# Kernel tuning notes

Measured on AMD Instinct MI355X. Metric: run time of the kernel, lower is better.

The kernel has to match this reference:

```python
import jax
import jax.numpy as jnp
import numpy as np

T, B = 128, 64
A_DIM, Z_DIM, K_MIX = 32, 64, 16
HIDDEN, NUM_LAYERS = 128, 2
Q_REG = 1e-3
R_REG = 1e-3


def _lstm_layer(x, Wih, Whh, bih, bhh):
    # x: [T, B, in]; torch gate order i, f, g, o
    H = Whh.shape[1]
    h0 = jnp.zeros((x.shape[1], H), x.dtype)

    def step(carry, xt):
        h, c = carry
        gates = xt @ Wih.T + bih + h @ Whh.T + bhh
        i, f, g, o = jnp.split(gates, 4, axis=-1)
        c = jax.nn.sigmoid(f) * c + jax.nn.sigmoid(i) * jnp.tanh(g)
        h = jax.nn.sigmoid(o) * jnp.tanh(c)
        return (h, c), h

    _, hs = jax.lax.scan(step, (h0, h0), x)
    return hs


def _weights(as_, lstm_params, lin_W, lin_b):
    x = as_
    for (Wih, Whh, bih, bhh) in lstm_params:
        x = _lstm_layer(x, Wih, Whh, bih, bhh)
    logits = x @ lin_W.T + lin_b  # [T, B, K]
    return jax.nn.softmax(logits, axis=-1)


def setup_inputs() -> dict:
    key = jax.random.key(0)
    ks = jax.random.split(key, 16)
    inp = {
        "as_": jax.random.normal(ks[0], (T, B, A_DIM), jnp.float32),
        # 0.3 scale keeps the mixture transition matrix spectral radius < 1
        "mat_A_K": 0.3 * jax.random.normal(ks[1], (K_MIX, Z_DIM, Z_DIM), jnp.float32),
        "mat_C_K": jax.random.normal(ks[2], (K_MIX, A_DIM, Z_DIM), jnp.float32),
        "Q_L": jax.random.normal(ks[3], (Z_DIM, Z_DIM), jnp.float32),
        "R_L": jax.random.normal(ks[4], (A_DIM, A_DIM), jnp.float32),
        "lin_W": jax.random.normal(ks[5], (K_MIX, HIDDEN), jnp.float32) / np.sqrt(HIDDEN),
        "lin_b": jnp.zeros((K_MIX,), jnp.float32),
    }
    s = 1.0 / np.sqrt(HIDDEN)
    for l in range(NUM_LAYERS):
        in_dim = A_DIM if l == 0 else HIDDEN
        k1, k2 = jax.random.split(jax.random.fold_in(key, 100 + l))
        inp[f"lstm_Wih{l}"] = s * jax.random.normal(k1, (4 * HIDDEN, in_dim), jnp.float32)
        inp[f"lstm_Whh{l}"] = s * jax.random.normal(k2, (4 * HIDDEN, HIDDEN), jnp.float32)
        inp[f"lstm_bih{l}"] = jnp.zeros((4 * HIDDEN,), jnp.float32)
        inp[f"lstm_bhh{l}"] = jnp.zeros((4 * HIDDEN,), jnp.float32)
    return inp


def reference(as_, mat_A_K, mat_C_K, Q_L, R_L, lin_W, lin_b,
              lstm_Wih0, lstm_Whh0, lstm_bih0, lstm_bhh0,
              lstm_Wih1, lstm_Whh1, lstm_bih1, lstm_bhh1):
    lstm_params = [(lstm_Wih0, lstm_Whh0, lstm_bih0, lstm_bhh0),
                   (lstm_Wih1, lstm_Whh1, lstm_bih1, lstm_bhh1)]
    w = _weights(as_, lstm_params, lin_W, lin_b)            # [T, B, K]
    mat_As = jnp.einsum('tbk,kij->tbij', w, mat_A_K)         # [T, B, z, z]
    mat_Cs = jnp.einsum('tbk,kij->tbij', w, mat_C_K)         # [T, B, a, z]

    I_z = jnp.eye(Z_DIM, dtype=as_.dtype)
    I_a = jnp.eye(A_DIM, dtype=as_.dtype)
    Q = Q_L @ Q_L.T + Q_REG * I_z
    R = R_L @ R_L.T + R_REG * I_a

    mean0 = jnp.zeros((B, Z_DIM, 1), as_.dtype)              # initial_state_mean = 0
    cov0 = jnp.broadcast_to(I_z, (B, Z_DIM, Z_DIM))          # initial_state_covariance = I

    def sym(M):
        return 0.5 * (M + jnp.swapaxes(M, 1, 2))

    def step(carry, inp):
        mean_p, cov_p = carry
        A_t, C_t, a_t = inp                                   # [B,z,z], [B,a,z], [B,a]
        C_tT = jnp.swapaxes(C_t, 1, 2)
        S = C_t @ cov_p @ C_tT + R                            # [B, a, a]
        K_t = cov_p @ C_tT @ jnp.linalg.inv(S)                # [B, z, a]
        mean_t = mean_p + K_t @ (a_t[..., None] - C_t @ mean_p)
        mean_next = A_t @ mean_t
        cov_t = sym(cov_p - K_t @ C_t @ cov_p)
        cov_next = sym(A_t @ cov_t @ jnp.swapaxes(A_t, 1, 2) + Q)
        return (mean_next, cov_next), (mean_t, cov_t, mean_next, cov_next)

    _, (means, covs, next_means, next_covs) = jax.lax.scan(
        step, (mean0, cov0), (mat_As, mat_Cs, as_))
    return means, covs, next_means, next_covs, mat_As, mat_Cs
```

## Files before the change

kernel.cpp:

```cpp
#include <hip/hip_runtime.h>
#include <math.h>

#define T_LEN 128
#define B_SZ  64
#define AD    32
#define ZD    64
#define KMIX  16
#define HID   128

#define WS_B0 106496
#define WS_B1 107008
#define WS_Q  107520
#define WS_R  111616
#define WS_W  112640

#define OUT_MEANS   0
#define OUT_COVS    524288
#define OUT_NMEANS  34078720
#define OUT_NCOVS   34603008
#define OUT_MATA    68157440
#define OUT_MATC    101711872

__device__ __forceinline__ float sigmoidf_(float x){ return 1.0f/(1.0f + expf(-x)); }

__device__ __forceinline__ unsigned short f2bf(float f){
  unsigned u = __float_as_uint(f);
  u += 0x7FFFu + ((u >> 16) & 1u);
  return (unsigned short)(u >> 16);
}

__global__ __launch_bounds__(256) void prep_kernel(
    const float* __restrict__ Wih0, const float* __restrict__ Whh0,
    const float* __restrict__ bih0, const float* __restrict__ bhh0,
    const float* __restrict__ Wih1, const float* __restrict__ Whh1,
    const float* __restrict__ bih1, const float* __restrict__ bhh1,
    const float* __restrict__ QL,   const float* __restrict__ RL,
    float* __restrict__ ws)
{
  int idx = blockIdx.x*256 + threadIdx.x;
  unsigned short* w16 = (unsigned short*)ws;
  if (idx < 212992) {
    const float* src; int local, base, IN;
    if (idx < 16384)       { src = Wih0; local = idx;          base = 0;      IN = 32; }
    else if (idx < 81920)  { src = Whh0; local = idx - 16384;  base = 16384;  IN = 128; }
    else if (idx < 147456) { src = Wih1; local = idx - 81920;  base = 81920;  IN = 128; }
    else                   { src = Whh1; local = idx - 147456; base = 147456; IN = 128; }
    int pair = local >> 10, g = (local >> 1) & 511, lo = local & 1;
    int k = pair*2 + lo;
    w16[base + local] = f2bf(src[g*IN + k]);
  } else if (idx < 213504) {
    int g = idx - 212992; ws[WS_B0 + g] = bih0[g] + bhh0[g];
  } else if (idx < 214016) {
    int g = idx - 213504; ws[WS_B1 + g] = bih1[g] + bhh1[g];
  } else if (idx < 218112) {
    int e = idx - 214016; int i = e >> 6, j = e & 63;
    float s = (i==j) ? 1e-3f : 0.f;
    for (int k = 0; k < 64; ++k) s += QL[i*64+k]*QL[j*64+k];
    ws[WS_Q + e] = s;
  } else if (idx < 219136) {
    int e = idx - 218112; int i = e >> 5, j = e & 31;
    float s = (i==j) ? 1e-3f : 0.f;
    for (int k = 0; k < 32; ++k) s += RL[i*32+k]*RL[j*32+k];
    ws[WS_R + e] = s;
  }
}

__global__ __launch_bounds__(1024) void lstm_kernel(
    const float* __restrict__ as_, const float* __restrict__ ws,
    const float* __restrict__ linW, const float* __restrict__ linb,
    float* __restrict__ wout)
{
  const int b = blockIdx.x, tid = threadIdx.x;
  const int g = tid & 511, hf = tid >> 9;
  const unsigned* W0ih = (const unsigned*)ws;
  const unsigned* W0hh = W0ih + 16*512;
  const unsigned* W1ih = W0hh + 64*512;
  const unsigned* W1hh = W1ih + 64*512;

  __shared__ float xs[2][32];
  __shared__ float h0[128];
  __shared__ float h1[128];
  __shared__ float gpart[2][512];
  __shared__ float lw[16*132];

  for (int e = tid; e < 2048; e += 1024) lw[(e >> 7)*132 + (e & 127)] = linW[e];
  if (tid < 128) { h0[tid] = 0.f; h1[tid] = 0.f; }
  if (tid < 32)  xs[0][tid] = as_[(0*B_SZ + b)*AD + tid];
  float c0 = 0.f, c1 = 0.f;
  const float bias0 = (hf == 0) ? ws[WS_B0 + g] : 0.f;
  const float bias1 = (hf == 0) ? ws[WS_B1 + g] : 0.f;
  const float lbk = linb[tid & 15];
  __syncthreads();

  for (int t = 0; t < T_LEN; ++t) {
    const int cp = t & 1, np = cp ^ 1;
    {
      float acc = bias0;
      const int k0i = hf*8, k0h = hf*32;
      #pragma unroll
      for (int kk = 0; kk < 8; ++kk) {
        const unsigned u = W0ih[(k0i+kk)*512 + g];
        acc += __uint_as_float(u << 16) * xs[cp][2*(k0i+kk)]
             + __uint_as_float(u & 0xFFFF0000u) * xs[cp][2*(k0i+kk)+1];
      }
      #pragma unroll 8
      for (int kk = 0; kk < 32; ++kk) {
        const unsigned u = W0hh[(k0h+kk)*512 + g];
        acc += __uint_as_float(u << 16) * h0[2*(k0h+kk)]
             + __uint_as_float(u & 0xFFFF0000u) * h0[2*(k0h+kk)+1];
      }
      gpart[hf][g] = acc;
    }
    __syncthreads();
    if (tid < 128) {
      float ig = sigmoidf_(gpart[0][tid]     + gpart[1][tid]);
      float fg = sigmoidf_(gpart[0][tid+128] + gpart[1][tid+128]);
      float gg = tanhf    (gpart[0][tid+256] + gpart[1][tid+256]);
      float og = sigmoidf_(gpart[0][tid+384] + gpart[1][tid+384]);
      c0 = fg*c0 + ig*gg;
      h0[tid] = og * tanhf(c0);
    } else if (tid >= 512 && tid < 544 && t+1 < T_LEN) {
      xs[np][tid-512] = as_[((t+1)*B_SZ + b)*AD + (tid-512)];
    }
    __syncthreads();
    {
      float acc = bias1;
      const int k0 = hf*32;
      #pragma unroll 8
      for (int kk = 0; kk < 32; ++kk) {
        const unsigned u = W1ih[(k0+kk)*512 + g];
        acc += __uint_as_float(u << 16) * h0[2*(k0+kk)]
             + __uint_as_float(u & 0xFFFF0000u) * h0[2*(k0+kk)+1];
      }
      #pragma unroll 8
      for (int kk = 0; kk < 32; ++kk) {
        const unsigned u = W1hh[(k0+kk)*512 + g];
        acc += __uint_as_float(u << 16) * h1[2*(k0+kk)]
             + __uint_as_float(u & 0xFFFF0000u) * h1[2*(k0+kk)+1];
      }
      gpart[hf][g] = acc;
    }
    __syncthreads();
    if (tid < 128) {
      float ig = sigmoidf_(gpart[0][tid]     + gpart[1][tid]);
      float fg = sigmoidf_(gpart[0][tid+128] + gpart[1][tid+128]);
      float gg = tanhf    (gpart[0][tid+256] + gpart[1][tid+256]);
      float og = sigmoidf_(gpart[0][tid+384] + gpart[1][tid+384]);
      c1 = fg*c1 + ig*gg;
      h1[tid] = og * tanhf(c1);
    }
    __syncthreads();
    if (tid < 64) {
      const int k = tid & 15, q = tid >> 4;
      float acc = 0.f;
      const float* lr = &lw[k*132 + q*32];
      const float* hr = &h1[q*32];
      #pragma unroll 8
      for (int j = 0; j < 32; ++j) acc += lr[j] * hr[j];
      acc += __shfl_xor(acc, 16);
      acc += __shfl_xor(acc, 32);
      const float logit = acc + lbk;
      float m = logit;
      m = fmaxf(m, __shfl_xor(m, 1));
      m = fmaxf(m, __shfl_xor(m, 2));
      m = fmaxf(m, __shfl_xor(m, 4));
      m = fmaxf(m, __shfl_xor(m, 8));
      const float e = expf(logit - m);
      float s = e;
      s += __shfl_xor(s, 1); s += __shfl_xor(s, 2);
      s += __shfl_xor(s, 4); s += __shfl_xor(s, 8);
      if (tid < 16) wout[(t*B_SZ + b)*KMIX + k] = e / s;
    }
  }
}

__global__ __launch_bounds__(256) void mix_kernel(
    const float* __restrict__ w, const float* __restrict__ AK,
    const float* __restrict__ CK, float* __restrict__ out)
{
  float* matA = out + OUT_MATA;
  float* matC = out + OUT_MATC;
  const int tb0 = blockIdx.x * 16;
  const int tid = threadIdx.x;
  __shared__ float wl[16][16];
  { int lt = tid >> 4, k = tid & 15; wl[lt][k] = w[(tb0 + lt)*16 + k]; }
  __syncthreads();

  for (int e = tid; e < ZD*ZD; e += 256) {
    float v[16];
    #pragma unroll
    for (int u = 0; u < 16; ++u) v[u] = 0.f;
    #pragma unroll 4
    for (int k = 0; k < 16; ++k) {
      float a = AK[k*ZD*ZD + e];
      #pragma unroll
      for (int u = 0; u < 16; ++u) v[u] += wl[u][k] * a;
    }
    #pragma unroll
    for (int u = 0; u < 16; ++u) matA[(size_t)(tb0+u)*(ZD*ZD) + e] = v[u];
  }
  for (int e = tid; e < AD*ZD; e += 256) {
    float v[16];
    #pragma unroll
    for (int u = 0; u < 16; ++u) v[u] = 0.f;
    #pragma unroll 4
    for (int k = 0; k < 16; ++k) {
      float a = CK[k*AD*ZD + e];
      #pragma unroll
      for (int u = 0; u < 16; ++u) v[u] += wl[u][k] * a;
    }
    #pragma unroll
    for (int u = 0; u < 16; ++u) matC[(size_t)(tb0+u)*(AD*ZD) + e] = v[u];
  }
}

__global__ __launch_bounds__(512, 1) void kalman_kernel(
    const float* __restrict__ as_, const float* __restrict__ ws,
    float* __restrict__ out)
{
  const int b = blockIdx.x, tid = threadIdx.x;
  const float* Rm = ws + WS_R;
  const float* Qg = ws + WS_Q;
  const float* matA = out + OUT_MATA;
  const float* matC = out + OUT_MATC;
  float* means  = out + OUT_MEANS;
  float* covs   = out + OUT_COVS;
  float* nmeans = out + OUT_NMEANS;
  float* ncovs  = out + OUT_NCOVS;

  __shared__ __align__(16) float covp[64*68];
  __shared__ __align__(16) float At[2][64*68];
  __shared__ __align__(16) float Cm[2][32*68];
  __shared__ __align__(16) float CPm[32*68];
  __shared__ __align__(16) float Wm[32*68];
  __shared__ float Smat[32*36];
  __shared__ __align__(16) float Um[64*68];
  __shared__ __align__(16) float Vt[32*68];

  for (int e = tid; e < 64*68; e += 512) covp[e] = 0.f;
  __syncthreads();
  for (int e = tid; e < 64*64; e += 512) {
    const int i = e >> 6, j = e & 63;
    covp[i*68 + j] = (i == j) ? 1.f : 0.f;
  }
  float4 qr0, qr1;
  {
    const int i2 = (tid >> 4)*2, j0 = (tid & 15)*4;
    qr0 = *(const float4*)&Qg[(i2+0)*64 + j0];
    qr1 = *(const float4*)&Qg[(i2+1)*64 + j0];
  }
  {
    const float* Ag = matA + (size_t)b*4096;
    const float* Cg = matC + (size_t)b*2048;
    for (int e = tid; e < 4096; e += 512) At[0][(e & 63)*68 + (e >> 6)] = Ag[e];
    for (int e = tid; e < 2048; e += 512) Cm[0][(e >> 6)*68 + (e & 63)] = Cg[e];
  }
  __syncthreads();

  int cur = 0;
  for (int t = 0; t < T_LEN; ++t) {
    const int tb = t*B_SZ + b;
    const int nxt = cur ^ 1;

    if (tid < 256) {
      const int i2 = (tid >> 4)*2, j0 = (tid & 15)*4;
      const bool do64 = ((tid & 15) == 15);
      const float* Cr0 = &Cm[cur][(i2+0)*68];
      const float* Cr1 = &Cm[cur][(i2+1)*68];
      float4 accA = make_float4(0,0,0,0), accB = accA;
      float s64a = 0.f, s64b = 0.f;
      #pragma unroll 4
      for (int k4 = 0; k4 < 16; ++k4) {
        const float4 a4 = *(const float4*)&Cr0[k4*4];
        const float4 c4 = *(const float4*)&Cr1[k4*4];
        const float4 b0 = *(const float4*)&covp[(k4*4+0)*68 + j0];
        const float4 b1 = *(const float4*)&covp[(k4*4+1)*68 + j0];
        const float4 b2 = *(const float4*)&covp[(k4*4+2)*68 + j0];
        const float4 b3 = *(const float4*)&covp[(k4*4+3)*68 + j0];
        accA.x += a4.x*b0.x + a4.y*b1.x + a4.z*b2.x + a4.w*b3.x;
        accA.y += a4.x*b0.y + a4.y*b1.y + a4.z*b2.y + a4.w*b3.y;
        accA.z += a4.x*b0.z + a4.y*b1.z + a4.z*b2.z + a4.w*b3.z;
        accA.w += a4.x*b0.w + a4.y*b1.w + a4.z*b2.w + a4.w*b3.w;
        accB.x += c4.x*b0.x + c4.y*b1.x + c4.z*b2.x + c4.w*b3.x;
        accB.y += c4.x*b0.y + c4.y*b1.y + c4.z*b2.y + c4.w*b3.y;
        accB.z += c4.x*b0.z + c4.y*b1.z + c4.z*b2.z + c4.w*b3.z;
        accB.w += c4.x*b0.w + c4.y*b1.w + c4.z*b2.w + c4.w*b3.w;
        if (do64) {
          const float m0 = covp[(k4*4+0)*68+64], m1 = covp[(k4*4+1)*68+64];
          const float m2 = covp[(k4*4+2)*68+64], m3 = covp[(k4*4+3)*68+64];
          s64a += a4.x*m0 + a4.y*m1 + a4.z*m2 + a4.w*m3;
          s64b += c4.x*m0 + c4.y*m1 + c4.z*m2 + c4.w*m3;
        }
      }
      *(float4*)&CPm[(i2+0)*68 + j0] = accA;
      *(float4*)&CPm[(i2+1)*68 + j0] = accB;
      if (do64) {
        const float2 av = *(const float2*)&as_[(size_t)tb*AD + i2];
        CPm[(i2+0)*68 + 64] = s64a - av.x;
        CPm[(i2+1)*68 + 64] = s64b - av.y;
      }
    }
    __syncthreads();
    if (tid < 256) {
      const int i2 = (tid >> 4)*2, j2 = (tid & 15)*2;
      const float* cpr0 = &CPm[(i2+0)*68];
      const float* cpr1 = &CPm[(i2+1)*68];
      const float* cr0  = &Cm[cur][(j2+0)*68];
      const float* cr1  = &Cm[cur][(j2+1)*68];
      float s00=0,s01=0,s10=0,s11=0;
      #pragma unroll 4
      for (int k4 = 0; k4 < 16; ++k4) {
        const float4 p0 = *(const float4*)&cpr0[k4*4];
        const float4 p1 = *(const float4*)&cpr1[k4*4];
        const float4 c0 = *(const float4*)&cr0[k4*4];
        const float4 c1 = *(const float4*)&cr1[k4*4];
        s00 += p0.x*c0.x + p0.y*c0.y + p0.z*c0.z + p0.w*c0.w;
        s01 += p0.x*c1.x + p0.y*c1.y + p0.z*c1.z + p0.w*c1.w;
        s10 += p1.x*c0.x + p1.y*c0.y + p1.z*c0.z + p1.w*c0.w;
        s11 += p1.x*c1.x + p1.y*c1.y + p1.z*c1.z + p1.w*c1.w;
      }
      Smat[(i2+0)*36 + j2+0] = s00 + Rm[(i2+0)*32 + j2+0];
      Smat[(i2+0)*36 + j2+1] = s01 + Rm[(i2+0)*32 + j2+1];
      Smat[(i2+1)*36 + j2+0] = s10 + Rm[(i2+1)*32 + j2+0];
      Smat[(i2+1)*36 + j2+1] = s11 + Rm[(i2+1)*32 + j2+1];
    }
    __syncthreads();
    {
      const int wv = tid >> 6, lane = tid & 63;
      if (wv == 0) {
        if (lane < 32) {
          float Lr[32];
          float invd = 0.f;
          #pragma unroll
          for (int j = 0; j < 32; ++j) Lr[j] = Smat[lane*36 + j];
          #pragma unroll
          for (int k = 0; k < 32; ++k) {
            const float piv = __shfl(Lr[k], k);
            const float ir  = 1.0f / sqrtf(piv);
            const float lik = Lr[k] * ir;
            invd = (lane == k) ? ir : invd;
            #pragma unroll
            for (int j = k+1; j < 32; ++j) {
              const float ljk = __shfl(lik, j);
              Lr[j] -= lik * ljk;
            }
            Lr[k] = lik;
          }
          #pragma unroll
          for (int j = 0; j < 32; ++j)
            if (j < lane) Smat[lane*36 + j] = Lr[j];
          Smat[lane*36 + lane] = invd;
        }
      } else {
        const int su = tid - 64;
        const int row2 = (su & 31)*2, g = su >> 5;
        const int q0c = g*4, q1c = (g+14)*4;
        const float* Atc = At[cur];
        float4 acc0 = make_float4(0,0,0,0), acc1 = acc0, acc2 = acc0, acc3 = acc0;
        #pragma unroll 8
        for (int k = 0; k < 64; ++k) {
          const float2 a2 = *(const float2*)&Atc[k*68 + row2];
          const float4 b0 = *(const float4*)&covp[k*68 + q0c];
          acc0.x += a2.x*b0.x; acc0.y += a2.x*b0.y; acc0.z += a2.x*b0.z; acc0.w += a2.x*b0.w;
          acc1.x += a2.y*b0.x; acc1.y += a2.y*b0.y; acc1.z += a2.y*b0.z; acc1.w += a2.y*b0.w;
          if (g < 3) {
            const float4 b1 = *(const float4*)&covp[k*68 + q1c];
            acc2.x += a2.x*b1.x; acc2.y += a2.x*b1.y; acc2.z += a2.x*b1.z; acc2.w += a2.x*b1.w;
            acc3.x += a2.y*b1.x; acc3.y += a2.y*b1.y; acc3.z += a2.y*b1.z; acc3.w += a2.y*b1.w;
          }
        }
        *(float4*)&Um[(row2+0)*68 + q0c] = acc0;
        *(float4*)&Um[(row2+1)*68 + q0c] = acc1;
        if (g < 3) {
          *(float4*)&Um[(row2+0)*68 + q1c] = acc2;
          *(float4*)&Um[(row2+1)*68 + q1c] = acc3;
        }
      }
    }
    __syncthreads();
    {
      if (tid < 65) {
        const int c = tid;
        float s[32];
        #pragma unroll
        for (int i = 0; i < 32; ++i) s[i] = CPm[i*68 + c];
        #pragma unroll
        for (int k = 0; k < 32; ++k) {
          const float y = s[k] * Smat[k*36 + k];
          Wm[k*68 + c] = y;
          #pragma unroll
          for (int i = k+1; i < 32; ++i)
            s[i] -= Smat[i*36 + k] * y;
        }
      } else if (tid >= 128 && t < T_LEN-1) {
        const int su = tid - 128;
        const float* Ag = matA + (size_t)(tb+64)*4096;
        const float* Cg = matC + (size_t)(tb+64)*2048;
        const float4 q0 = *(const float4*)&Ag[su*4];
        const float4 q1 = *(const float4*)&Ag[(su+384)*4];
        const float4 q2 = (su < 256) ? *(const float4*)&Ag[(su+768)*4]
                                     : *(const float4*)&Cg[(su-256)*4];
        const float4 q3 = *(const float4*)&Cg[(su+128)*4];
        { const int c = su;       const int i = c>>4, j = (c&15)*4;
          At[nxt][(j+0)*68+i]=q0.x; At[nxt][(j+1)*68+i]=q0.y; At[nxt][(j+2)*68+i]=q0.z; At[nxt][(j+3)*68+i]=q0.w; }
        { const int c = su + 384; const int i = c>>4, j = (c&15)*4;
          At[nxt][(j+0)*68+i]=q1.x; At[nxt][(j+1)*68+i]=q1.y; At[nxt][(j+2)*68+i]=q1.z; At[nxt][(j+3)*68+i]=q1.w; }
        if (su < 256) { const int c = su + 768; const int i = c>>4, j = (c&15)*4;
          At[nxt][(j+0)*68+i]=q2.x; At[nxt][(j+1)*68+i]=q2.y; At[nxt][(j+2)*68+i]=q2.z; At[nxt][(j+3)*68+i]=q2.w; }
        else { const int cc = su - 256; *(float4*)&Cm[nxt][(cc>>4)*68 + (cc&15)*4] = q2; }
        { const int cc = su + 128;      *(float4*)&Cm[nxt][(cc>>4)*68 + (cc&15)*4] = q3; }
      }
    }
    __syncthreads();
    if (tid < 256) {
      const int j2 = (tid >> 3)*2, c0 = (tid & 7)*8;
      const bool do64 = ((tid & 7) == 7);
      float4 a0 = make_float4(0,0,0,0), a1 = a0, b0a = a0, b1a = a0;
      float s64a = 0.f, s64b = 0.f;
      #pragma unroll 8
      for (int k = 0; k < 32; ++k) {
        const float2 w2 = *(const float2*)&Wm[k*68 + j2];
        const float4 q0 = *(const float4*)&Wm[k*68 + c0];
        const float4 q1 = *(const float4*)&Wm[k*68 + c0 + 4];
        a0.x += w2.x*q0.x; a0.y += w2.x*q0.y; a0.z += w2.x*q0.z; a0.w += w2.x*q0.w;
        a1.x += w2.x*q1.x; a1.y += w2.x*q1.y; a1.z += w2.x*q1.z; a1.w += w2.x*q1.w;
        b0a.x += w2.y*q0.x; b0a.y += w2.y*q0.y; b0a.z += w2.y*q0.z; b0a.w += w2.y*q0.w;
        b1a.x += w2.y*q1.x; b1a.y += w2.y*q1.y; b1a.z += w2.y*q1.z; b1a.w += w2.y*q1.w;
        if (do64) { const float wm = Wm[k*68 + 64]; s64a += w2.x*wm; s64b += w2.y*wm; }
      }
      float4 c0a = *(const float4*)&covp[(j2+0)*68 + c0];
      float4 c0b = *(const float4*)&covp[(j2+0)*68 + c0 + 4];
      float4 c1a = *(const float4*)&covp[(j2+1)*68 + c0];
      float4 c1b = *(const float4*)&covp[(j2+1)*68 + c0 + 4];
      c0a.x -= a0.x;  c0a.y -= a0.y;  c0a.z -= a0.z;  c0a.w -= a0.w;
      c0b.x -= a1.x;  c0b.y -= a1.y;  c0b.z -= a1.z;  c0b.w -= a1.w;
      c1a.x -= b0a.x; c1a.y -= b0a.y; c1a.z -= b0a.z; c1a.w -= b0a.w;
      c1b.x -= b1a.x; c1b.y -= b1a.y; c1b.z -= b1a.z; c1b.w -= b1a.w;
      *(float4*)&covs[(size_t)tb*4096 + (j2+0)*64 + c0]     = c0a;
      *(float4*)&covs[(size_t)tb*4096 + (j2+0)*64 + c0 + 4] = c0b;
      *(float4*)&covs[(size_t)tb*4096 + (j2+1)*64 + c0]     = c1a;
      *(float4*)&covs[(size_t)tb*4096 + (j2+1)*64 + c0 + 4] = c1b;
      if (do64) {
        means[(size_t)tb*64 + j2+0] = covp[(j2+0)*68 + 64] - s64a;
        means[(size_t)tb*64 + j2+1] = covp[(j2+1)*68 + 64] - s64b;
      }
    } else {
      const int task = tid - 256;
      const int a2 = (task >> 4)*2, c0 = (task & 15)*4;
      const float* Wr0 = &Wm[(a2+0)*68];
      const float* Wr1 = &Wm[(a2+1)*68];
      const float* Atc = At[cur];
      float4 acc0 = make_float4(0,0,0,0), acc1 = acc0;
      #pragma unroll 4
      for (int k4 = 0; k4 < 16; ++k4) {
        const float4 w0 = *(const float4*)&Wr0[k4*4];
        const float4 w1 = *(const float4*)&Wr1[k4*4];
        const float4 b0 = *(const float4*)&Atc[(k4*4+0)*68 + c0];
        const float4 b1 = *(const float4*)&Atc[(k4*4+1)*68 + c0];
        const float4 b2 = *(const float4*)&Atc[(k4*4+2)*68 + c0];
        const float4 b3 = *(const float4*)&Atc[(k4*4+3)*68 + c0];
        acc0.x += w0.x*b0.x + w0.y*b1.x + w0.z*b2.x + w0.w*b3.x;
        acc0.y += w0.x*b0.y + w0.y*b1.y + w0.z*b2.y + w0.w*b3.y;
        acc0.z += w0.x*b0.z + w0.y*b1.z + w0.z*b2.z + w0.w*b3.z;
        acc0.w += w0.x*b0.w + w0.y*b1.w + w0.z*b2.w + w0.w*b3.w;
        acc1.x += w1.x*b0.x + w1.y*b1.x + w1.z*b2.x + w1.w*b3.x;
        acc1.y += w1.x*b0.y + w1.y*b1.y + w1.z*b2.y + w1.w*b3.y;
        acc1.z += w1.x*b0.z + w1.y*b1.z + w1.z*b2.z + w1.w*b3.z;
        acc1.w += w1.x*b0.w + w1.y*b1.w + w1.z*b2.w + w1.w*b3.w;
      }
      *(float4*)&Vt[(a2+0)*68 + c0] = acc0;
      *(float4*)&Vt[(a2+1)*68 + c0] = acc1;
    }
    __syncthreads();
    {
      const int i2 = (tid >> 4)*2, j0 = (tid & 15)*4;
      const float* Atc = At[cur];
      const float* u0 = &Um[(i2+0)*68];
      const float* u1 = &Um[(i2+1)*68];
      float4 a0 = qr0;
      float4 a1 = qr1;
      #pragma unroll 4
      for (int k4 = 0; k4 < 16; ++k4) {
        const float4 t0 = *(const float4*)&u0[k4*4];
        const float4 t1 = *(const float4*)&u1[k4*4];
        #pragma unroll
        for (int m = 0; m < 4; ++m) {
          const float av0 = (m==0)?t0.x:(m==1)?t0.y:(m==2)?t0.z:t0.w;
          const float av1 = (m==0)?t1.x:(m==1)?t1.y:(m==2)?t1.z:t1.w;
          const float4 bb = *(const float4*)&Atc[(k4*4+m)*68 + j0];
          a0.x += av0*bb.x; a0.y += av0*bb.y; a0.z += av0*bb.z; a0.w += av0*bb.w;
          a1.x += av1*bb.x; a1.y += av1*bb.y; a1.z += av1*bb.z; a1.w += av1*bb.w;
        }
      }
      #pragma unroll 8
      for (int a = 0; a < 32; ++a) {
        const float2 v2 = *(const float2*)&Vt[a*68 + i2];
        const float4 bb = *(const float4*)&Vt[a*68 + j0];
        a0.x -= v2.x*bb.x; a0.y -= v2.x*bb.y; a0.z -= v2.x*bb.z; a0.w -= v2.x*bb.w;
        a1.x -= v2.y*bb.x; a1.y -= v2.y*bb.y; a1.z -= v2.y*bb.z; a1.w -= v2.y*bb.w;
      }
      *(float4*)&covp[(i2+0)*68 + j0] = a0;
      *(float4*)&covp[(i2+1)*68 + j0] = a1;
      *(float4*)&ncovs[(size_t)tb*4096 + (i2+0)*64 + j0] = a0;
      *(float4*)&ncovs[(size_t)tb*4096 + (i2+1)*64 + j0] = a1;
      if ((tid & 15) == 15) {
        float s64a = Um[(i2+0)*68 + 64];
        float s64b = Um[(i2+1)*68 + 64];
        #pragma unroll 8
        for (int a = 0; a < 32; ++a) {
          const float2 v2 = *(const float2*)&Vt[a*68 + i2];
          const float wm = Wm[a*68 + 64];
          s64a -= v2.x*wm; s64b -= v2.y*wm;
        }
        covp[(i2+0)*68 + 64] = s64a;
        covp[(i2+1)*68 + 64] = s64b;
        nmeans[(size_t)tb*64 + i2+0] = s64a;
        nmeans[(size_t)tb*64 + i2+1] = s64b;
      }
    }
    __syncthreads();
    cur = nxt;
  }
}

extern "C" void kernel_launch(void* const* d_in, const int* in_sizes, int n_in,
                              void* d_out, int out_size, void* d_ws, size_t ws_size,
                              hipStream_t stream) {
  const float* as_  = (const float*)d_in[0];
  const float* AK   = (const float*)d_in[1];
  const float* CK   = (const float*)d_in[2];
  const float* QL   = (const float*)d_in[3];
  const float* RL   = (const float*)d_in[4];
  const float* linW = (const float*)d_in[5];
  const float* linb = (const float*)d_in[6];
  const float* Wih0 = (const float*)d_in[7];
  const float* Whh0 = (const float*)d_in[8];
  const float* bih0 = (const float*)d_in[9];
  const float* bhh0 = (const float*)d_in[10];
  const float* Wih1 = (const float*)d_in[11];
  const float* Whh1 = (const float*)d_in[12];
  const float* bih1 = (const float*)d_in[13];
  const float* bhh1 = (const float*)d_in[14];
  float* out = (float*)d_out;
  float* ws  = (float*)d_ws;

  prep_kernel<<<856, 256, 0, stream>>>(Wih0, Whh0, bih0, bhh0,
                                       Wih1, Whh1, bih1, bhh1, QL, RL, ws);
  lstm_kernel<<<B_SZ, 1024, 0, stream>>>(as_, ws, linW, linb, ws + WS_W);
  mix_kernel<<<(T_LEN*B_SZ)/16, 256, 0, stream>>>(ws + WS_W, AK, CK, out);
  kalman_kernel<<<B_SZ, 512, 0, stream>>>(as_, ws, out);
}
```

Measured before the change: 3.847 ms.

## Use 4x4 register tiles and split mean-column work into dedicated threads

Rewrites the per-step Kalman matmuls (C·P, S, A·P, W·W, W·A, and the covariance update) to give each thread a 4x4 or 4x8 register tile instead of 2xN, so fewer threads do more arithmetic per shared-memory load. The augmented mean column (index 64) no longer goes through the divergent do64 branches in the main tiles; dedicated small thread groups compute it, with a separate mcol vector carrying the mean. Q moves into shared memory instead of being held in registers. This cuts LDS traffic per FMA and removes branch divergence, but fewer threads are active per phase, which may expose latency inside this serial per-batch recurrence.

```diff
diff --git a/kernel.cpp b/kernel.cpp
--- a/kernel.cpp
+++ b/kernel.cpp
@@ -28,6 +28,9 @@
   u += 0x7FFFu + ((u >> 16) & 1u);
   return (unsigned short)(u >> 16);
 }
+
+#define F4FMA(acc, s, v) { (acc).x += (s)*(v).x; (acc).y += (s)*(v).y; (acc).z += (s)*(v).z; (acc).w += (s)*(v).w; }
+#define F4FMS(acc, s, v) { (acc).x -= (s)*(v).x; (acc).y -= (s)*(v).y; (acc).z -= (s)*(v).z; (acc).w -= (s)*(v).w; }
 
 __global__ __launch_bounds__(256) void prep_kernel(
     const float* __restrict__ Wih0, const float* __restrict__ Whh0,
@@ -236,19 +239,17 @@
   __shared__ float Smat[32*36];
   __shared__ __align__(16) float Um[64*68];
   __shared__ __align__(16) float Vt[32*68];
+  __shared__ __align__(16) float Ql[64*68];
+  __shared__ __align__(16) float mcol[64];
 
   for (int e = tid; e < 64*68; e += 512) covp[e] = 0.f;
   __syncthreads();
   for (int e = tid; e < 64*64; e += 512) {
     const int i = e >> 6, j = e & 63;
+    Ql[i*68 + j]   = Qg[e];
     covp[i*68 + j] = (i == j) ? 1.f : 0.f;
   }
-  float4 qr0, qr1;
-  {
-    const int i2 = (tid >> 4)*2, j0 = (tid & 15)*4;
-    qr0 = *(const float4*)&Qg[(i2+0)*64 + j0];
-    qr1 = *(const float4*)&Qg[(i2+1)*64 + j0];
-  }
+  if (tid < 64) mcol[tid] = 0.f;
   {
     const float* Ag = matA + (size_t)b*4096;
     const float* Cg = matC + (size_t)b*2048;
@@ -262,67 +263,82 @@
     const int tb = t*B_SZ + b;
     const int nxt = cur ^ 1;
 
-    if (tid < 256) {
-      const int i2 = (tid >> 4)*2, j0 = (tid & 15)*4;
-      const bool do64 = ((tid & 15) == 15);
-      const float* Cr0 = &Cm[cur][(i2+0)*68];
-      const float* Cr1 = &Cm[cur][(i2+1)*68];
-      float4 accA = make_float4(0,0,0,0), accB = accA;
-      float s64a = 0.f, s64b = 0.f;
+    if (tid < 128) {
+      const int i0 = (tid >> 4)*4, j0 = (tid & 15)*4;
+      const float* Cb = Cm[cur];
+      float4 a0 = make_float4(0,0,0,0), a1 = a0, a2 = a0, a3 = a0;
       #pragma unroll 4
       for (int k4 = 0; k4 < 16; ++k4) {
-        const float4 a4 = *(const float4*)&Cr0[k4*4];
-        const float4 c4 = *(const float4*)&Cr1[k4*4];
-        const float4 b0 = *(const float4*)&covp[(k4*4+0)*68 + j0];
-        const float4 b1 = *(const float4*)&covp[(k4*4+1)*68 + j0];
-        const float4 b2 = *(const float4*)&covp[(k4*4+2)*68 + j0];
-        const float4 b3 = *(const float4*)&covp[(k4*4+3)*68 + j0];
-        accA.x += a4.x*b0.x + a4.y*b1.x + a4.z*b2.x + a4.w*b3.x;
-        accA.y += a4.x*b0.y + a4.y*b1.y + a4.z*b2.y + a4.w*b3.y;
-        accA.z += a4.x*b0.z + a4.y*b1.z + a4.z*b2.z + a4.w*b3.z;
-        accA.w += a4.x*b0.w + a4.y*b1.w + a4.z*b2.w + a4.w*b3.w;
-        accB.x += c4.x*b0.x + c4.y*b1.x + c4.z*b2.x + c4.w*b3.x;
-        accB.y += c4.x*b0.y + c4.y*b1.y + c4.z*b2.y + c4.w*b3.y;
-        accB.z += c4.x*b0.z + c4.y*b1.z + c4.z*b2.z + c4.w*b3.z;
-        accB.w += c4.x*b0.w + c4.y*b1.w + c4.z*b2.w + c4.w*b3.w;
-        if (do64) {
-          const float m0 = covp[(k4*4+0)*68+64], m1 = covp[(k4*4+1)*68+64];
-          const float m2 = covp[(k4*4+2)*68+64], m3 = covp[(k4*4+3)*68+64];
-          s64a += a4.x*m0 + a4.y*m1 + a4.z*m2 + a4.w*m3;
-          s64b += c4.x*m0 + c4.y*m1 + c4.z*m2 + c4.w*m3;
-        }
-      }
-      *(float4*)&CPm[(i2+0)*68 + j0] = accA;
-      *(float4*)&CPm[(i2+1)*68 + j0] = accB;
-      if (do64) {
-        const float2 av = *(const float2*)&as_[(size_t)tb*AD + i2];
-        CPm[(i2+0)*68 + 64] = s64a - av.x;
-        CPm[(i2+1)*68 + 64] = s64b - av.y;
-      }
-    }
-    __syncthreads();
-    if (tid < 256) {
-      const int i2 = (tid >> 4)*2, j2 = (tid & 15)*2;
-      const float* cpr0 = &CPm[(i2+0)*68];
-      const float* cpr1 = &CPm[(i2+1)*68];
-      const float* cr0  = &Cm[cur][(j2+0)*68];
-      const float* cr1  = &Cm[cur][(j2+1)*68];
-      float s00=0,s01=0,s10=0,s11=0;
+        const int k = k4*4;
+        const float4 c0 = *(const float4*)&Cb[(i0+0)*68 + k];
+        const float4 c1 = *(const float4*)&Cb[(i0+1)*68 + k];
+        const float4 c2 = *(const float4*)&Cb[(i0+2)*68 + k];
+        const float4 c3 = *(const float4*)&Cb[(i0+3)*68 + k];
+        const float4 b0 = *(const float4*)&covp[(k+0)*68 + j0];
+        const float4 b1 = *(const float4*)&covp[(k+1)*68 + j0];
+        const float4 b2 = *(const float4*)&covp[(k+2)*68 + j0];
+        const float4 b3 = *(const float4*)&covp[(k+3)*68 + j0];
+        F4FMA(a0, c0.x, b0) F4FMA(a0, c0.y, b1) F4FMA(a0, c0.z, b2) F4FMA(a0, c0.w, b3)
+        F4FMA(a1, c1.x, b0) F4FMA(a1, c1.y, b1) F4FMA(a1, c1.z, b2) F4FMA(a1, c1.w, b3)
+        F4FMA(a2, c2.x, b0) F4FMA(a2, c2.y, b1) F4FMA(a2, c2.z, b2) F4FMA(a2, c2.w, b3)
+        F4FMA(a3, c3.x, b0) F4FMA(a3, c3.y, b1) F4FMA(a3, c3.z, b2) F4FMA(a3, c3.w, b3)
+      }
+      *(float4*)&CPm[(i0+0)*68 + j0] = a0;
+      *(float4*)&CPm[(i0+1)*68 + j0] = a1;
+      *(float4*)&CPm[(i0+2)*68 + j0] = a2;
+      *(float4*)&CPm[(i0+3)*68 + j0] = a3;
+    } else if (tid < 160) {
+      const int i = tid - 128;
+      const float* Crow = &Cm[cur][i*68];
+      float s = -as_[(size_t)tb*AD + i];
       #pragma unroll 4
       for (int k4 = 0; k4 < 16; ++k4) {
-        const float4 p0 = *(const float4*)&cpr0[k4*4];
-        const float4 p1 = *(const float4*)&cpr1[k4*4];
-        const float4 c0 = *(const float4*)&cr0[k4*4];
-        const float4 c1 = *(const float4*)&cr1[k4*4];
-        s00 += p0.x*c0.x + p0.y*c0.y + p0.z*c0.z + p0.w*c0.w;
-        s01 += p0.x*c1.x + p0.y*c1.y + p0.z*c1.z + p0.w*c1.w;
-        s10 += p1.x*c0.x + p1.y*c0.y + p1.z*c0.z + p1.w*c0.w;
-        s11 += p1.x*c1.x + p1.y*c1.y + p1.z*c1.z + p1.w*c1.w;
-      }
-      Smat[(i2+0)*36 + j2+0] = s00 + Rm[(i2+0)*32 + j2+0];
-      Smat[(i2+0)*36 + j2+1] = s01 + Rm[(i2+0)*32 + j2+1];
-      Smat[(i2+1)*36 + j2+0] = s10 + Rm[(i2+1)*32 + j2+0];
-      Smat[(i2+1)*36 + j2+1] = s11 + Rm[(i2+1)*32 + j2+1];
+        const float4 c4 = *(const float4*)&Crow[k4*4];
+        const float4 m4 = *(const float4*)&mcol[k4*4];
+        s += c4.x*m4.x + c4.y*m4.y + c4.z*m4.z + c4.w*m4.w;
+      }
+      CPm[i*68 + 64] = s;
+    }
+    __syncthreads();
+    if (tid < 64) {
+      const int i0 = (tid >> 3)*4, j0 = (tid & 7)*4;
+      float4 a0 = make_float4(0,0,0,0), a1 = a0, a2 = a0, a3 = a0;
+      #pragma unroll 4
+      for (int k4 = 0; k4 < 16; ++k4) {
+        const int k = k4*4;
+        const float4 p0 = *(const float4*)&CPm[(i0+0)*68 + k];
+        const float4 p1 = *(const float4*)&CPm[(i0+1)*68 + k];
+        const float4 p2 = *(const float4*)&CPm[(i0+2)*68 + k];
+        const float4 p3 = *(const float4*)&CPm[(i0+3)*68 + k];
+        const float4 c0 = *(const float4*)&Cm[cur][(j0+0)*68 + k];
+        const float4 c1 = *(const float4*)&Cm[cur][(j0+1)*68 + k];
+        const float4 c2 = *(const float4*)&Cm[cur][(j0+2)*68 + k];
+        const float4 c3 = *(const float4*)&Cm[cur][(j0+3)*68 + k];
+        a0.x += p0.x*c0.x + p0.y*c0.y + p0.z*c0.z + p0.w*c0.w;
+        a0.y += p0.x*c1.x + p0.y*c1.y + p0.z*c1.z + p0.w*c1.w;
+        a0.z += p0.x*c2.x + p0.y*c2.y + p0.z*c2.z + p0.w*c2.w;
+        a0.w += p0.x*c3.x + p0.y*c3.y + p0.z*c3.z + p0.w*c3.w;
+        a1.x += p1.x*c0.x + p1.y*c0.y + p1.z*c0.z + p1.w*c0.w;
+        a1.y += p1.x*c1.x + p1.y*c1.y + p1.z*c1.z + p1.w*c1.w;
+        a1.z += p1.x*c2.x + p1.y*c2.y + p1.z*c2.z + p1.w*c2.w;
+        a1.w += p1.x*c3.x + p1.y*c3.y + p1.z*c3.z + p1.w*c3.w;
+        a2.x += p2.x*c0.x + p2.y*c0.y + p2.z*c0.z + p2.w*c0.w;
+        a2.y += p2.x*c1.x + p2.y*c1.y + p2.z*c1.z + p2.w*c1.w;
+        a2.z += p2.x*c2.x + p2.y*c2.y + p2.z*c2.z + p2.w*c2.w;
+        a2.w += p2.x*c3.x + p2.y*c3.y + p2.z*c3.z + p2.w*c3.w;
+        a3.x += p3.x*c0.x + p3.y*c0.y + p3.z*c0.z + p3.w*c0.w;
+        a3.y += p3.x*c1.x + p3.y*c1.y + p3.z*c1.z + p3.w*c1.w;
+        a3.z += p3.x*c2.x + p3.y*c2.y + p3.z*c2.z + p3.w*c2.w;
+        a3.w += p3.x*c3.x + p3.y*c3.y + p3.z*c3.z + p3.w*c3.w;
+      }
+      #pragma unroll
+      for (int r = 0; r < 4; ++r) {
+        const float4 av = (r==0)?a0:(r==1)?a1:(r==2)?a2:a3;
+        Smat[(i0+r)*36 + j0+0] = av.x + Rm[(i0+r)*32 + j0+0];
+        Smat[(i0+r)*36 + j0+1] = av.y + Rm[(i0+r)*32 + j0+1];
+        Smat[(i0+r)*36 + j0+2] = av.z + Rm[(i0+r)*32 + j0+2];
+        Smat[(i0+r)*36 + j0+3] = av.w + Rm[(i0+r)*32 + j0+3];
+      }
     }
     __syncthreads();
     {
@@ -351,30 +367,46 @@
             if (j < lane) Smat[lane*36 + j] = Lr[j];
           Smat[lane*36 + lane] = invd;
         }
-      } else {
-        const int su = tid - 64;
-        const int row2 = (su & 31)*2, g = su >> 5;
-        const int q0c = g*4, q1c = (g+14)*4;
+      } else if (tid < 192) {
+        const int u = tid - 64;
+        const int r0 = (u >> 3)*4, qa = (u & 7)*4, qb = qa + 32;
         const float* Atc = At[cur];
-        float4 acc0 = make_float4(0,0,0,0), acc1 = acc0, acc2 = acc0, acc3 = acc0;
+        float4 pa0 = make_float4(0,0,0,0), pa1 = pa0, pa2 = pa0, pa3 = pa0;
+        float4 pb0 = pa0, pb1 = pa0, pb2 = pa0, pb3 = pa0;
         #pragma unroll 8
         for (int k = 0; k < 64; ++k) {
-          const float2 a2 = *(const float2*)&Atc[k*68 + row2];
-          const float4 b0 = *(const float4*)&covp[k*68 + q0c];
-          acc0.x += a2.x*b0.x; acc0.y += a2.x*b0.y; acc0.z += a2.x*b0.z; acc0.w += a2.x*b0.w;
-          acc1.x += a2.y*b0.x; acc1.y += a2.y*b0.y; acc1.z += a2.y*b0.z; acc1.w += a2.y*b0.w;
-          if (g < 3) {
-            const float4 b1 = *(const float4*)&covp[k*68 + q1c];
-            acc2.x += a2.x*b1.x; acc2.y += a2.x*b1.y; acc2.z += a2.x*b1.z; acc2.w += a2.x*b1.w;
-            acc3.x += a2.y*b1.x; acc3.y += a2.y*b1.y; acc3.z += a2.y*b1.z; acc3.w += a2.y*b1.w;
+          const float4 av = *(const float4*)&Atc[k*68 + r0];
+          const float4 b0 = *(const float4*)&covp[k*68 + qa];
+          const float4 b1 = *(const float4*)&covp[k*68 + qb];
+          F4FMA(pa0, av.x, b0) F4FMA(pa1, av.y, b0) F4FMA(pa2, av.z, b0) F4FMA(pa3, av.w, b0)
+          F4FMA(pb0, av.x, b1) F4FMA(pb1, av.y, b1) F4FMA(pb2, av.z, b1) F4FMA(pb3, av.w, b1)
+        }
+        *(float4*)&Um[(r0+0)*68 + qa] = pa0;
+        *(float4*)&Um[(r0+1)*68 + qa] = pa1;
+        *(float4*)&Um[(r0+2)*68 + qa] = pa2;
+        *(float4*)&Um[(r0+3)*68 + qa] = pa3;
+        *(float4*)&Um[(r0+0)*68 + qb] = pb0;
+        *(float4*)&Um[(r0+1)*68 + qb] = pb1;
+        *(float4*)&Um[(r0+2)*68 + qb] = pb2;
+        *(float4*)&Um[(r0+3)*68 + qb] = pb3;
+      } else if (tid < 208) {
+        const int r0 = (tid - 192)*4;
+        const float* Atc = At[cur];
+        float s0=0.f, s1=0.f, s2=0.f, s3=0.f;
+        #pragma unroll 4
+        for (int k4 = 0; k4 < 16; ++k4) {
+          const float4 m4 = *(const float4*)&mcol[k4*4];
+          #pragma unroll
+          for (int m = 0; m < 4; ++m) {
+            const float mk = (m==0)?m4.x:(m==1)?m4.y:(m==2)?m4.z:m4.w;
+            const float4 av = *(const float4*)&Atc[(k4*4+m)*68 + r0];
+            s0 += av.x*mk; s1 += av.y*mk; s2 += av.z*mk; s3 += av.w*mk;
           }
         }
-        *(float4*)&Um[(row2+0)*68 + q0c] = acc0;
-        *(float4*)&Um[(row2+1)*68 + q0c] = acc1;
-        if (g < 3) {
-          *(float4*)&Um[(row2+0)*68 + q1c] = acc2;
-          *(float4*)&Um[(row2+1)*68 + q1c] = acc3;
-        }
+        Um[(r0+0)*68 + 64] = s0;
+        Um[(r0+1)*68 + 64] = s1;
+        Um[(r0+2)*68 + 64] = s2;
+        Um[(r0+3)*68 + 64] = s3;
       }
     }
     __syncthreads();
@@ -412,111 +444,140 @@
       }
     }
     __syncthreads();
-    if (tid < 256) {
-      const int j2 = (tid >> 3)*2, c0 = (tid & 7)*8;
-      const bool do64 = ((tid & 7) == 7);
-      float4 a0 = make_float4(0,0,0,0), a1 = a0, b0a = a0, b1a = a0;
-      float s64a = 0.f, s64b = 0.f;
+    if (tid < 128) {
+      const int j0 = (tid >> 3)*4, c0 = (tid & 7)*8;
+      float4 x00 = make_float4(0,0,0,0), x01 = x00, x10 = x00, x11 = x00;
+      float4 x20 = x00, x21 = x00, x30 = x00, x31 = x00;
       #pragma unroll 8
       for (int k = 0; k < 32; ++k) {
-        const float2 w2 = *(const float2*)&Wm[k*68 + j2];
-        const float4 q0 = *(const float4*)&Wm[k*68 + c0];
-        const float4 q1 = *(const float4*)&Wm[k*68 + c0 + 4];
-        a0.x += w2.x*q0.x; a0.y += w2.x*q0.y; a0.z += w2.x*q0.z; a0.w += w2.x*q0.w;
-        a1.x += w2.x*q1.x; a1.y += w2.x*q1.y; a1.z += w2.x*q1.z; a1.w += w2.x*q1.w;
-        b0a.x += w2.y*q0.x; b0a.y += w2.y*q0.y; b0a.z += w2.y*q0.z; b0a.w += w2.y*q0.w;
-        b1a.x += w2.y*q1.x; b1a.y += w2.y*q1.y; b1a.z += w2.y*q1.z; b1a.w += w2.y*q1.w;
-        if (do64) { const float wm = Wm[k*68 + 64]; s64a += w2.x*wm; s64b += w2.y*wm; }
-      }
-      float4 c0a = *(const float4*)&covp[(j2+0)*68 + c0];
-      float4 c0b = *(const float4*)&covp[(j2+0)*68 + c0 + 4];
-      float4 c1a = *(const float4*)&covp[(j2+1)*68 + c0];
-      float4 c1b = *(const float4*)&covp[(j2+1)*68 + c0 + 4];
-      c0a.x -= a0.x;  c0a.y -= a0.y;  c0a.z -= a0.z;  c0a.w -= a0.w;
-      c0b.x -= a1.x;  c0b.y -= a1.y;  c0b.z -= a1.z;  c0b.w -= a1.w;
-      c1a.x -= b0a.x; c1a.y -= b0a.y; c1a.z -= b0a.z; c1a.w -= b0a.w;
-      c1b.x -= b1a.x; c1b.y -= b1a.y; c1b.z -= b1a.z; c1b.w -= b1a.w;
-      *(float4*)&covs[(size_t)tb*4096 + (j2+0)*64 + c0]     = c0a;
-      *(float4*)&covs[(size_t)tb*4096 + (j2+0)*64 + c0 + 4] = c0b;
-      *(float4*)&covs[(size_t)tb*4096 + (j2+1)*64 + c0]     = c1a;
-      *(float4*)&covs[(size_t)tb*4096 + (j2+1)*64 + c0 + 4] = c1b;
-      if (do64) {
-        means[(size_t)tb*64 + j2+0] = covp[(j2+0)*68 + 64] - s64a;
-        means[(size_t)tb*64 + j2+1] = covp[(j2+1)*68 + 64] - s64b;
-      }
-    } else {
-      const int task = tid - 256;
-      const int a2 = (task >> 4)*2, c0 = (task & 15)*4;
-      const float* Wr0 = &Wm[(a2+0)*68];
-      const float* Wr1 = &Wm[(a2+1)*68];
+        const float4 wj = *(const float4*)&Wm[k*68 + j0];
+        const float4 qa = *(const float4*)&Wm[k*68 + c0];
+        const float4 qb = *(const float4*)&Wm[k*68 + c0 + 4];
+        F4FMA(x00, wj.x, qa) F4FMA(x01, wj.x, qb)
+        F4FMA(x10, wj.y, qa) F4FMA(x11, wj.y, qb)
+        F4FMA(x20, wj.z, qa) F4FMA(x21, wj.z, qb)
+        F4FMA(x30, wj.w, qa) F4FMA(x31, wj.w, qb)
+      }
+      #pragma unroll
+      for (int r = 0; r < 4; ++r) {
+        const float4 xa = (r==0)?x00:(r==1)?x10:(r==2)?x20:x30;
+        const float4 xb = (r==0)?x01:(r==1)?x11:(r==2)?x21:x31;
+        float4 ca = *(const float4*)&covp[(j0+r)*68 + c0];
+        float4 cb = *(const float4*)&covp[(j0+r)*68 + c0 + 4];
+        ca.x -= xa.x; ca.y -= xa.y; ca.z -= xa.z; ca.w -= xa.w;
+        cb.x -= xb.x; cb.y -= xb.y; cb.z -= xb.z; cb.w -= xb.w;
+        *(float4*)&covs[(size_t)tb*4096 + (j0+r)*64 + c0]     = ca;
+        *(float4*)&covs[(size_t)tb*4096 + (j0+r)*64 + c0 + 4] = cb;
+      }
+    } else if (tid < 144) {
+      const int i0 = (tid - 128)*4;
+      float s0=0.f, s1=0.f, s2=0.f, s3=0.f;
+      #pragma unroll 8
+      for (int k = 0; k < 32; ++k) {
+        const float4 wi = *(const float4*)&Wm[k*68 + i0];
+        const float wm = Wm[k*68 + 64];
+        s0 += wi.x*wm; s1 += wi.y*wm; s2 += wi.z*wm; s3 += wi.w*wm;
+      }
+      float4 mo;
+      mo.x = covp[(i0+0)*68 + 64] - s0;
+      mo.y = covp[(i0+1)*68 + 64] - s1;
+      mo.z = covp[(i0+2)*68 + 64] - s2;
+      mo.w = covp[(i0+3)*68 + 64] - s3;
+      *(float4*)&means[(size_t)tb*64 + i0] = mo;
+    } else if (tid >= 256 && tid < 320) {
+      const int v = tid - 256;
+      const int a0 = (v >> 3)*4, c0 = (v & 7)*8;
       const float* Atc = At[cur];
-      float4 acc0 = make_float4(0,0,0,0), acc1 = acc0;
+      float4 y00 = make_float4(0,0,0,0), y01 = y00, y10 = y00, y11 = y00;
+      float4 y20 = y00, y21 = y00, y30 = y00, y31 = y00;
       #pragma unroll 4
       for (int k4 = 0; k4 < 16; ++k4) {
-        const float4 w0 = *(const float4*)&Wr0[k4*4];
-        const float4 w1 = *(const float4*)&Wr1[k4*4];
-        const float4 b0 = *(const float4*)&Atc[(k4*4+0)*68 + c0];
-        const float4 b1 = *(const float4*)&Atc[(k4*4+1)*68 + c0];
-        const float4 b2 = *(const float4*)&Atc[(k4*4+2)*68 + c0];
-        const float4 b3 = *(const float4*)&Atc[(k4*4+3)*68 + c0];
-        acc0.x += w0.x*b0.x + w0.y*b1.x + w0.z*b2.x + w0.w*b3.x;
-        acc0.y += w0.x*b0.y + w0.y*b1.y + w0.z*b2.y + w0.w*b3.y;
-        acc0.z += w0.x*b0.z + w0.y*b1.z + w0.z*b2.z + w0.w*b3.z;
-        acc0.w += w0.x*b0.w + w0.y*b1.w + w0.z*b2.w + w0.w*b3.w;
-        acc1.x += w1.x*b0.x + w1.y*b1.x + w1.z*b2.x + w1.w*b3.x;
-        acc1.y += w1.x*b0.y + w1.y*b1.y + w1.z*b2.y + w1.w*b3.y;
-        acc1.z += w1.x*b0.z + w1.y*b1.z + w1.z*b2.z + w1.w*b3.z;
-        acc1.w += w1.x*b0.w + w1.y*b1.w + w1.z*b2.w + w1.w*b3.w;
-      }
-      *(float4*)&Vt[(a2+0)*68 + c0] = acc0;
-      *(float4*)&Vt[(a2+1)*68 + c0] = acc1;
-    }
-    __syncthreads();
-    {
-      const int i2 = (tid >> 4)*2, j0 = (tid & 15)*4;
+        const int k = k4*4;
+        const float4 w0 = *(const float4*)&Wm[(a0+0)*68 + k];
+        const float4 w1 = *(const float4*)&Wm[(a0+1)*68 + k];
+        const float4 w2 = *(const float4*)&Wm[(a0+2)*68 + k];
+        const float4 w3 = *(const float4*)&Wm[(a0+3)*68 + k];
+        #pragma unroll
+        for (int m = 0; m < 4; ++m) {
+          const float4 ta = *(const float4*)&Atc[(k+m)*68 + c0];
+          const float4 tb2 = *(const float4*)&Atc[(k+m)*68 + c0 + 4];
+          const float w0m = (m==0)?w0.x:(m==1)?w0.y:(m==2)?w0.z:w0.w;
+          const float w1m = (m==0)?w1.x:(m==1)?w1.y:(m==2)?w1.z:w1.w;
+          const float w2m = (m==0)?w2.x:(m==1)?w2.y:(m==2)?w2.z:w2.w;
+          const float w3m = (m==0)?w3.x:(m==1)?w3.y:(m==2)?w3.z:w3.w;
+          F4FMA(y00, w0m, ta) F4FMA(y01, w0m, tb2)
+          F4FMA(y10, w1m, ta) F4FMA(y11, w1m, tb2)
+          F4FMA(y20, w2m, ta) F4FMA(y21, w2m, tb2)
+          F4FMA(y30, w3m, ta) F4FMA(y31, w3m, tb2)
+        }
+      }
+      *(float4*)&Vt[(a0+0)*68 + c0]     = y00;
+      *(float4*)&Vt[(a0+0)*68 + c0 + 4] = y01;
+      *(float4*)&Vt[(a0+1)*68 + c0]     = y10;
+      *(float4*)&Vt[(a0+1)*68 + c0 + 4] = y11;
+      *(float4*)&Vt[(a0+2)*68 + c0]     = y20;
+      *(float4*)&Vt[(a0+2)*68 + c0 + 4] = y21;
+      *(float4*)&Vt[(a0+3)*68 + c0]     = y30;
+      *(float4*)&Vt[(a0+3)*68 + c0 + 4] = y31;
+    }
+    __syncthreads();
+    if (tid < 256) {
+      const int i0 = (tid >> 4)*4, j0 = (tid & 15)*4;
       const float* Atc = At[cur];
-      const float* u0 = &Um[(i2+0)*68];
-      const float* u1 = &Um[(i2+1)*68];
-      float4 a0 = qr0;
-      float4 a1 = qr1;
+      float4 a0 = *(const float4*)&Ql[(i0+0)*68 + j0];
+      float4 a1 = *(const float4*)&Ql[(i0+1)*68 + j0];
+      float4 a2 = *(const float4*)&Ql[(i0+2)*68 + j0];
+      float4 a3 = *(const float4*)&Ql[(i0+3)*68 + j0];
       #pragma unroll 4
       for (int k4 = 0; k4 < 16; ++k4) {
-        const float4 t0 = *(const float4*)&u0[k4*4];
-        const float4 t1 = *(const float4*)&u1[k4*4];
+        const int k = k4*4;
+        const float4 u0 = *(const float4*)&Um[(i0+0)*68 + k];
+        const float4 u1 = *(const float4*)&Um[(i0+1)*68 + k];
+        const float4 u2 = *(const float4*)&Um[(i0+2)*68 + k];
+        const float4 u3 = *(const float4*)&Um[(i0+3)*68 + k];
         #pragma unroll
         for (int m = 0; m < 4; ++m) {
-          const float av0 = (m==0)?t0.x:(m==1)?t0.y:(m==2)?t0.z:t0.w;
-          const float av1 = (m==0)?t1.x:(m==1)?t1.y:(m==2)?t1.z:t1.w;
-          const float4 bb = *(const float4*)&Atc[(k4*4+m)*68 + j0];
-          a0.x += av0*bb.x; a0.y += av0*bb.y; a0.z += av0*bb.z; a0.w += av0*bb.w;
-          a1.x += av1*bb.x; a1.y += av1*bb.y; a1.z += av1*bb.z; a1.w += av1*bb.w;
+          const float4 at = *(const float4*)&Atc[(k+m)*68 + j0];
+          const float u0m = (m==0)?u0.x:(m==1)?u0.y:(m==2)?u0.z:u0.w;
+          const float u1m = (m==0)?u1.x:(m==1)?u1.y:(m==2)?u1.z:u1.w;
+          const float u2m = (m==0)?u2.x:(m==1)?u2.y:(m==2)?u2.z:u2.w;
+          const float u3m = (m==0)?u3.x:(m==1)?u3.y:(m==2)?u3.z:u3.w;
+          F4FMA(a0, u0m, at) F4FMA(a1, u1m, at) F4FMA(a2, u2m, at) F4FMA(a3, u3m, at)
         }
       }
       #pragma unroll 8
       for (int a = 0; a < 32; ++a) {
-        const float2 v2 = *(const float2*)&Vt[a*68 + i2];
-        const float4 bb = *(const float4*)&Vt[a*68 + j0];
-        a0.x -= v2.x*bb.x; a0.y -= v2.x*bb.y; a0.z -= v2.x*bb.z; a0.w -= v2.x*bb.w;
-        a1.x -= v2.y*bb.x; a1.y -= v2.y*bb.y; a1.z -= v2.y*bb.z; a1.w -= v2.y*bb.w;
-      }
-      *(float4*)&covp[(i2+0)*68 + j0] = a0;
-      *(float4*)&covp[(i2+1)*68 + j0] = a1;
-      *(float4*)&ncovs[(size_t)tb*4096 + (i2+0)*64 + j0] = a0;
-      *(float4*)&ncovs[(size_t)tb*4096 + (i2+1)*64 + j0] = a1;
-      if ((tid & 15) == 15) {
-        float s64a = Um[(i2+0)*68 + 64];
-        float s64b = Um[(i2+1)*68 + 64];
-        #pragma unroll 8
-        for (int a = 0; a < 32; ++a) {
-          const float2 v2 = *(const float2*)&Vt[a*68 + i2];
-          const float wm = Wm[a*68 + 64];
-          s64a -= v2.x*wm; s64b -= v2.y*wm;
-        }
-        covp[(i2+0)*68 + 64] = s64a;
-        covp[(i2+1)*68 + 64] = s64b;
-        nmeans[(size_t)tb*64 + i2+0] = s64a;
-        nmeans[(size_t)tb*64 + i2+1] = s64b;
-      }
+        const float4 vi = *(const float4*)&Vt[a*68 + i0];
+        const float4 vj = *(const float4*)&Vt[a*68 + j0];
+        F4FMS(a0, vi.x, vj) F4FMS(a1, vi.y, vj) F4FMS(a2, vi.z, vj) F4FMS(a3, vi.w, vj)
+      }
+      *(float4*)&covp[(i0+0)*68 + j0] = a0;
+      *(float4*)&covp[(i0+1)*68 + j0] = a1;
+      *(float4*)&covp[(i0+2)*68 + j0] = a2;
+      *(float4*)&covp[(i0+3)*68 + j0] = a3;
+      *(float4*)&ncovs[(size_t)tb*4096 + (i0+0)*64 + j0] = a0;
+      *(float4*)&ncovs[(size_t)tb*4096 + (i0+1)*64 + j0] = a1;
+      *(float4*)&ncovs[(size_t)tb*4096 + (i0+2)*64 + j0] = a2;
+      *(float4*)&ncovs[(size_t)tb*4096 + (i0+3)*64 + j0] = a3;
+    } else if (tid < 272) {
+      const int i0 = (tid - 256)*4;
+      float s0 = Um[(i0+0)*68 + 64];
+      float s1 = Um[(i0+1)*68 + 64];
+      float s2 = Um[(i0+2)*68 + 64];
+      float s3 = Um[(i0+3)*68 + 64];
+      #pragma unroll 8
+      for (int a = 0; a < 32; ++a) {
+        const float4 vi = *(const float4*)&Vt[a*68 + i0];
+        const float wm = Wm[a*68 + 64];
+        s0 -= vi.x*wm; s1 -= vi.y*wm; s2 -= vi.z*wm; s3 -= vi.w*wm;
+      }
+      covp[(i0+0)*68 + 64] = s0;
+      covp[(i0+1)*68 + 64] = s1;
+      covp[(i0+2)*68 + 64] = s2;
+      covp[(i0+3)*68 + 64] = s3;
+      float4 mo = make_float4(s0, s1, s2, s3);
+      *(float4*)&mcol[i0] = mo;
+      *(float4*)&nmeans[(size_t)tb*64 + i0] = mo;
     }
     __syncthreads();
     cur = nxt;
```

After: 4.207 ms. +9.4%, slower.
